# Kernel optimization log

Measured on AMD Instinct MI355X. Metric: run time of the kernel, lower is better.

The kernel has to match this reference:

```python
import jax, jax.numpy as jnp
import numpy as np

D_MODEL = 1024
NUM_HEAD = 16
D_K = D_MODEL // NUM_HEAD


def setup_inputs() -> dict:
    key = jax.random.key(0)
    ks = jax.random.split(key, 9)
    s = 1.0 / np.sqrt(D_MODEL)
    return {
        "x": jax.random.normal(ks[0], (2, 2048, D_MODEL), dtype=jnp.float32),
        "Wq": jax.random.normal(ks[1], (D_MODEL, D_MODEL), dtype=jnp.float32) * s,
        "bq": jax.random.normal(ks[2], (D_MODEL,), dtype=jnp.float32) * s,
        "Wk": jax.random.normal(ks[3], (D_MODEL, D_MODEL), dtype=jnp.float32) * s,
        "bk": jax.random.normal(ks[4], (D_MODEL,), dtype=jnp.float32) * s,
        "Wv": jax.random.normal(ks[5], (D_MODEL, D_MODEL), dtype=jnp.float32) * s,
        "bv": jax.random.normal(ks[6], (D_MODEL,), dtype=jnp.float32) * s,
        "Wo": jax.random.normal(ks[7], (D_MODEL, D_MODEL), dtype=jnp.float32) * s,
        "bo": jax.random.normal(ks[8], (D_MODEL,), dtype=jnp.float32) * s,
    }


def reference(x, Wq, bq, Wk, bk, Wv, bv, Wo, bo):
    B, S, _ = x.shape
    # QKV projections: [B,S,D] -> [B,H,S,d_k]
    def proj(W, b):
        y = jnp.einsum("bsd,df->bsf", x, W) + b
        return y.reshape(B, S, NUM_HEAD, D_K).transpose(0, 2, 1, 3)

    Q = proj(Wq, bq)
    K = proj(Wk, bk)
    V = proj(Wv, bv)
    scale = 1.0 / jnp.sqrt(jnp.asarray(D_K, dtype=x.dtype))
    attn = jnp.einsum("bhqd,bhkd->bhqk", Q, K) * scale  # [B,H,S,S]
    probs = jax.nn.softmax(attn, axis=-1)
    out = jnp.einsum("bhqk,bhkd->bhqd", probs, V)  # [B,H,S,d_k]
    out = out.transpose(0, 2, 1, 3).reshape(B, S, D_MODEL)
    return jnp.einsum("bsd,df->bsf", out, Wo) + bo
```

## Files before the change

kernel.cpp:

```cpp
#include <hip/hip_runtime.h>
#include <hip/hip_bf16.h>
#include <math.h>

constexpr int DM = 1024;
constexpr int NH = 16;
constexpr int DK = 64;
constexpr int SQ = 2048;
constexpr int BB = 2;
constexpr int MR = BB * SQ;

typedef short bf16x8 __attribute__((ext_vector_type(8)));
typedef float f32x4 __attribute__((ext_vector_type(4)));

__device__ inline unsigned short f2bf(float f) {
  unsigned u = __float_as_uint(f);
  unsigned r = (u + 0x7fffu + ((u >> 16) & 1u)) >> 16;
  return (unsigned short)r;
}

__device__ inline int fswz(int r) { return (r & 7) ^ ((r >> 3) & 7); }
__device__ inline int swz(int r, int c) {
  return r * 64 + ((((c >> 3) ^ fswz(r)) & 7) << 3) + (c & 7);
}

__global__ __launch_bounds__(256)
void cast_kernel(const float* __restrict__ in, unsigned short* __restrict__ out, int n8) {
  int i = blockIdx.x * 256 + threadIdx.x;
  if (i >= n8) return;
  float4 a = *(const float4*)&in[(size_t)i * 8];
  float4 b = *(const float4*)&in[(size_t)i * 8 + 4];
  ushort4 lo = {f2bf(a.x), f2bf(a.y), f2bf(a.z), f2bf(a.w)};
  ushort4 hi = {f2bf(b.x), f2bf(b.y), f2bf(b.z), f2bf(b.w)};
  *(ushort4*)&out[(size_t)i * 8] = lo;
  *(ushort4*)&out[(size_t)i * 8 + 4] = hi;
}

__global__ __launch_bounds__(256)
void transpose_cast_kernel(const float* __restrict__ W, unsigned short* __restrict__ Wt) {
  __shared__ float tl[32][33];
  const int tx = threadIdx.x & 31, ty = threadIdx.x >> 5;
  const int x0 = blockIdx.x * 32, y0 = blockIdx.y * 32;
  #pragma unroll
  for (int i = 0; i < 4; ++i)
    tl[ty + i * 8][tx] = W[(size_t)(y0 + ty + i * 8) * DM + x0 + tx];
  __syncthreads();
  #pragma unroll
  for (int i = 0; i < 4; ++i)
    Wt[(size_t)(x0 + ty + i * 8) * DM + y0 + tx] = f2bf(tl[tx][ty + i * 8]);
}

__global__ __launch_bounds__(256)
void concat_bias(const float* __restrict__ bq, const float* __restrict__ bk,
                 const float* __restrict__ bv, float* __restrict__ cb) {
  int i = blockIdx.x * 256 + threadIdx.x;
  if (i < 1024) cb[i] = bq[i];
  else if (i < 2048) cb[i] = bk[i - 1024];
  else if (i < 3072) cb[i] = bv[i - 2048];
}

__global__ __launch_bounds__(256)
void qkv_gemm(const unsigned short* __restrict__ A, const unsigned short* __restrict__ Wt3,
              const float* __restrict__ cbias, unsigned short* __restrict__ qkv)
{
  constexpr int K = DM;
  __shared__ unsigned short As[2][128 * 64];
  __shared__ unsigned short Bs[2][128 * 64];
  const int t = threadIdx.x;
  const int w = t >> 6, ln = t & 63;
  const int wr = w >> 1, wc = w & 1;
  const int rb = blockIdx.y * 128, cb = blockIdx.x * 128;

  f32x4 acc[4][4] = {};

  auto stage = [&](int buf, int k0) {
    #pragma unroll
    for (int j = 0; j < 4; ++j) {
      const int rows8 = (w * 4 + j) * 8;
      const int r = rows8 + (ln >> 3);
      const int gc = (((ln & 7) ^ fswz(r)) & 7) * 8;
      __builtin_amdgcn_global_load_lds(
          (const __attribute__((address_space(1))) void*)&A[(size_t)(rb + r) * K + k0 + gc],
          (__attribute__((address_space(3))) void*)&As[buf][rows8 * 64], 16, 0, 0);
      __builtin_amdgcn_global_load_lds(
          (const __attribute__((address_space(1))) void*)&Wt3[(size_t)(cb + r) * K + k0 + gc],
          (__attribute__((address_space(3))) void*)&Bs[buf][rows8 * 64], 16, 0, 0);
    }
  };

  stage(0, 0);
  asm volatile("s_waitcnt vmcnt(0)" ::: "memory");
  __builtin_amdgcn_s_barrier();

  for (int it = 0; it < K / 64; ++it) {
    const int buf = it & 1;
    if (it < K / 64 - 1) stage(buf ^ 1, (it + 1) * 64);
    const int rsel = ln & 15;
    #pragma unroll
    for (int kk = 0; kk < 2; ++kk) {
      const int ko = kk * 32 + (ln >> 4) * 8;
      bf16x8 af[4], bfr[4];
      #pragma unroll
      for (int m = 0; m < 4; ++m)
        af[m] = *(const bf16x8*)&As[buf][swz(wr * 64 + m * 16 + rsel, ko)];
      #pragma unroll
      for (int n = 0; n < 4; ++n)
        bfr[n] = *(const bf16x8*)&Bs[buf][swz(wc * 64 + n * 16 + rsel, ko)];
      #pragma unroll
      for (int m = 0; m < 4; ++m)
        #pragma unroll
        for (int n = 0; n < 4; ++n)
          acc[m][n] = __builtin_amdgcn_mfma_f32_16x16x32_bf16(af[m], bfr[n], acc[m][n], 0, 0, 0);
    }
    asm volatile("s_waitcnt vmcnt(0)" ::: "memory");
    __builtin_amdgcn_s_barrier();
  }

  const int cl = ln & 15, rg = (ln >> 4) * 4;
  const int which = cb >> 10;
  const float sc = (which == 0) ? 0.125f : 1.0f;
  unsigned short* dst0 = qkv + (size_t)which * MR * DM;
  #pragma unroll
  for (int m = 0; m < 4; ++m) {
    #pragma unroll
    for (int i = 0; i < 4; ++i) {
      const int r = rb + wr * 64 + m * 16 + rg + i;
      const int b = r >> 11, s = r & 2047;
      #pragma unroll
      for (int n = 0; n < 4; ++n) {
        const int c = cb + wc * 64 + n * 16 + cl;
        const float v = (acc[m][n][i] + cbias[c]) * sc;
        const int cc = c & 1023, h = cc >> 6, d = c & 63;
        dst0[(((size_t)(b * NH + h)) * SQ + s) * DK + d] = f2bf(v);
      }
    }
  }
}

__global__ __launch_bounds__(256)
void mfma_gemm_out(const unsigned short* __restrict__ A, const unsigned short* __restrict__ Bt,
                   const float* __restrict__ bias, float* __restrict__ outp)
{
  constexpr int K = DM, N = DM;
  __shared__ unsigned short As[2][128 * 64];
  __shared__ unsigned short Bs[2][128 * 64];
  const int t = threadIdx.x;
  const int w = t >> 6, ln = t & 63;
  const int wr = w >> 1, wc = w & 1;
  const int rb = blockIdx.y * 128, cb = blockIdx.x * 128;

  f32x4 acc[4][4] = {};

  auto stage = [&](int buf, int k0) {
    #pragma unroll
    for (int j = 0; j < 4; ++j) {
      const int rows8 = (w * 4 + j) * 8;
      const int r = rows8 + (ln >> 3);
      const int gc = (((ln & 7) ^ fswz(r)) & 7) * 8;
      __builtin_amdgcn_global_load_lds(
          (const __attribute__((address_space(1))) void*)&A[(size_t)(rb + r) * K + k0 + gc],
          (__attribute__((address_space(3))) void*)&As[buf][rows8 * 64], 16, 0, 0);
      __builtin_amdgcn_global_load_lds(
          (const __attribute__((address_space(1))) void*)&Bt[(size_t)(cb + r) * K + k0 + gc],
          (__attribute__((address_space(3))) void*)&Bs[buf][rows8 * 64], 16, 0, 0);
    }
  };

  stage(0, 0);
  asm volatile("s_waitcnt vmcnt(0)" ::: "memory");
  __builtin_amdgcn_s_barrier();

  for (int it = 0; it < K / 64; ++it) {
    const int buf = it & 1;
    if (it < K / 64 - 1) stage(buf ^ 1, (it + 1) * 64);
    const int rsel = ln & 15;
    #pragma unroll
    for (int kk = 0; kk < 2; ++kk) {
      const int ko = kk * 32 + (ln >> 4) * 8;
      bf16x8 af[4], bfr[4];
      #pragma unroll
      for (int m = 0; m < 4; ++m)
        af[m] = *(const bf16x8*)&As[buf][swz(wr * 64 + m * 16 + rsel, ko)];
      #pragma unroll
      for (int n = 0; n < 4; ++n)
        bfr[n] = *(const bf16x8*)&Bs[buf][swz(wc * 64 + n * 16 + rsel, ko)];
      #pragma unroll
      for (int m = 0; m < 4; ++m)
        #pragma unroll
        for (int n = 0; n < 4; ++n)
          acc[m][n] = __builtin_amdgcn_mfma_f32_16x16x32_bf16(af[m], bfr[n], acc[m][n], 0, 0, 0);
    }
    asm volatile("s_waitcnt vmcnt(0)" ::: "memory");
    __builtin_amdgcn_s_barrier();
  }

  const int cl = ln & 15, rg = (ln >> 4) * 4;
  #pragma unroll
  for (int m = 0; m < 4; ++m) {
    #pragma unroll
    for (int i = 0; i < 4; ++i) {
      const int r = rb + wr * 64 + m * 16 + rg + i;
      #pragma unroll
      for (int n = 0; n < 4; ++n) {
        const int c = cb + wc * 64 + n * 16 + cl;
        outp[(size_t)r * N + c] = acc[m][n][i] + bias[c];
      }
    }
  }
}

__global__ __launch_bounds__(512, 4)
void attn_mfma(const unsigned short* __restrict__ Qp, const unsigned short* __restrict__ Kp,
               const unsigned short* __restrict__ Vp, unsigned short* __restrict__ ctx)
{
  __shared__ unsigned short Qs[128 * 64];
  __shared__ unsigned short Ks[2][64 * 64];
  __shared__ unsigned short Vt[2][64 * 64];
  __shared__ unsigned short Pl[8 * 16 * 64];
  const int t = threadIdx.x, w = t >> 6, ln = t & 63;
  const int bh = blockIdx.y, q0 = blockIdx.x * 128;
  const unsigned short* Qb = Qp + (size_t)bh * SQ * DK;
  const unsigned short* Kb = Kp + (size_t)bh * SQ * DK;
  const unsigned short* Vb = Vp + (size_t)bh * SQ * DK;

  #pragma unroll
  for (int i = 0; i < 2; ++i) {
    int g = t + i * 512, r = g >> 3, cg = g & 7;
    uint4 qv = *(const uint4*)&Qb[(size_t)(q0 + r) * DK + cg * 8];
    *(uint4*)&Qs[r * 64 + (((cg ^ fswz(r)) & 7) << 3)] = qv;
  }
  __syncthreads();
  const int rsel = ln & 15, ko = (ln >> 4) * 8;
  bf16x8 qf[2];
  #pragma unroll
  for (int kw = 0; kw < 2; ++kw)
    qf[kw] = *(const bf16x8*)&Qs[swz(w * 16 + rsel, ko + 32 * kw)];

  f32x4 acc2[4] = {};
  float m = -1e30f, l = 0.f;

  const int r0 = t >> 3, cg0 = t & 7;
  const int ksl = r0 * 64 + (((cg0 ^ fswz(r0)) & 7) << 3);
  {
    uint4 kg = *(const uint4*)&Kb[(size_t)r0 * DK + cg0 * 8];
    uint4 vg = *(const uint4*)&Vb[(size_t)r0 * DK + cg0 * 8];
    *(uint4*)&Ks[0][ksl] = kg;
    const unsigned short* vv = (const unsigned short*)&vg;
    #pragma unroll
    for (int e = 0; e < 8; ++e)
      Vt[0][swz(cg0 * 8 + e, r0)] = vv[e];
  }
  __syncthreads();

  int cur = 0;
  for (int c0 = 0; c0 < SQ; c0 += 64) {
    const bool haveNext = (c0 + 64 < SQ);
    uint4 kg, vg;
    if (haveNext) {
      kg = *(const uint4*)&Kb[(size_t)(c0 + 64 + r0) * DK + cg0 * 8];
      vg = *(const uint4*)&Vb[(size_t)(c0 + 64 + r0) * DK + cg0 * 8];
    }

    f32x4 s[4] = {};
    __builtin_amdgcn_s_setprio(1);
    #pragma unroll
    for (int kw = 0; kw < 2; ++kw)
      #pragma unroll
      for (int fr = 0; fr < 4; ++fr) {
        bf16x8 kf = *(const bf16x8*)&Ks[cur][swz(fr * 16 + rsel, ko + 32 * kw)];
        s[fr] = __builtin_amdgcn_mfma_f32_16x16x32_bf16(kf, qf[kw], s[fr], 0, 0, 0);
      }
    __builtin_amdgcn_s_setprio(0);

    float t0 = fmaxf(fmaxf(s[0][0], s[0][1]), fmaxf(s[0][2], s[0][3]));
    float t1 = fmaxf(fmaxf(s[1][0], s[1][1]), fmaxf(s[1][2], s[1][3]));
    float t2 = fmaxf(fmaxf(s[2][0], s[2][1]), fmaxf(s[2][2], s[2][3]));
    float t3 = fmaxf(fmaxf(s[3][0], s[3][1]), fmaxf(s[3][2], s[3][3]));
    float tm = fmaxf(fmaxf(t0, t1), fmaxf(t2, t3));
    tm = fmaxf(tm, __shfl_xor(tm, 16));
    tm = fmaxf(tm, __shfl_xor(tm, 32));

    if (__any((tm - m) > 8.f)) {
      const float mnew = fmaxf(m, tm);
      const float corr = __expf(m - mnew);
      float ci[4];
      #pragma unroll
      for (int i = 0; i < 4; ++i) ci[i] = __shfl(corr, (ln >> 4) * 4 + i);
      #pragma unroll
      for (int n = 0; n < 4; ++n)
        #pragma unroll
        for (int i = 0; i < 4; ++i) acc2[n][i] *= ci[i];
      l *= corr;
      m = mnew;
    }

    float p[4][4];
    #pragma unroll
    for (int fr = 0; fr < 4; ++fr)
      #pragma unroll
      for (int i = 0; i < 4; ++i)
        p[fr][i] = __expf(s[fr][i] - m);
    float a0 = (p[0][0] + p[0][1]) + (p[0][2] + p[0][3]);
    float a1 = (p[1][0] + p[1][1]) + (p[1][2] + p[1][3]);
    float a2 = (p[2][0] + p[2][1]) + (p[2][2] + p[2][3]);
    float a3 = (p[3][0] + p[3][1]) + (p[3][2] + p[3][3]);
    float ps = (a0 + a1) + (a2 + a3);
    ps += __shfl_xor(ps, 16);
    ps += __shfl_xor(ps, 32);
    l += ps;

    #pragma unroll
    for (int fr = 0; fr < 4; ++fr) {
      unsigned r01, r23;
      asm("v_cvt_pk_bf16_f32 %0, %1, %2" : "=v"(r01) : "v"(p[fr][0]), "v"(p[fr][1]));
      asm("v_cvt_pk_bf16_f32 %0, %1, %2" : "=v"(r23) : "v"(p[fr][2]), "v"(p[fr][3]));
      uint2 pv = {r01, r23};
      const int kk0 = (ln >> 4) * 4 + fr * 16;
      *(uint2*)&Pl[w * 1024 + swz(rsel, kk0)] = pv;
    }

    __builtin_amdgcn_s_setprio(1);
    #pragma unroll
    for (int kw = 0; kw < 2; ++kw) {
      bf16x8 pf = *(const bf16x8*)&Pl[w * 1024 + swz(rsel, ko + 32 * kw)];
      #pragma unroll
      for (int n = 0; n < 4; ++n) {
        bf16x8 vf = *(const bf16x8*)&Vt[cur][swz(n * 16 + rsel, ko + 32 * kw)];
        acc2[n] = __builtin_amdgcn_mfma_f32_16x16x32_bf16(pf, vf, acc2[n], 0, 0, 0);
      }
    }
    __builtin_amdgcn_s_setprio(0);

    if (haveNext) {
      *(uint4*)&Ks[cur ^ 1][ksl] = kg;
      const unsigned short* vv = (const unsigned short*)&vg;
      #pragma unroll
      for (int e = 0; e < 8; ++e)
        Vt[cur ^ 1][swz(cg0 * 8 + e, r0)] = vv[e];
      __syncthreads();
    }
    cur ^= 1;
  }

  const float rl = 1.0f / l;
  float ri[4];
  #pragma unroll
  for (int i = 0; i < 4; ++i) ri[i] = __shfl(rl, (ln >> 4) * 4 + i);
  const int b = bh >> 4, h = bh & 15;
  #pragma unroll
  for (int n = 0; n < 4; ++n)
    #pragma unroll
    for (int i = 0; i < 4; ++i) {
      const int srow = q0 + w * 16 + (ln >> 4) * 4 + i;
      ctx[((size_t)(b * SQ + srow)) * DM + h * 64 + n * 16 + rsel] =
          f2bf(acc2[n][i] * ri[i]);
    }
}

extern "C" void kernel_launch(void* const* d_in, const int* in_sizes, int n_in,
                              void* d_out, int out_size, void* d_ws, size_t ws_size,
                              hipStream_t stream) {
  const float* x  = (const float*)d_in[0];
  const float* Wq = (const float*)d_in[1];
  const float* bq = (const float*)d_in[2];
  const float* Wk = (const float*)d_in[3];
  const float* bk = (const float*)d_in[4];
  const float* Wv = (const float*)d_in[5];
  const float* bv = (const float*)d_in[6];
  const float* Wo = (const float*)d_in[7];
  const float* bo = (const float*)d_in[8];
  float* out = (float*)d_out;

  unsigned short* xb    = (unsigned short*)d_ws;
  unsigned short* Wt3   = xb   + (size_t)MR * DM;
  unsigned short* Wto   = Wt3  + (size_t)3 * DM * DM;
  unsigned short* QKVb  = Wto  + (size_t)DM * DM;
  unsigned short* ctxb  = QKVb + (size_t)3 * MR * DM;
  float*          cbias = (float*)(ctxb + (size_t)MR * DM);

  cast_kernel<<<(MR * DM / 8 + 255) / 256, 256, 0, stream>>>(x, xb, MR * DM / 8);
  dim3 tg(DM / 32, DM / 32);
  transpose_cast_kernel<<<tg, 256, 0, stream>>>(Wq, Wt3);
  transpose_cast_kernel<<<tg, 256, 0, stream>>>(Wk, Wt3 + (size_t)DM * DM);
  transpose_cast_kernel<<<tg, 256, 0, stream>>>(Wv, Wt3 + (size_t)2 * DM * DM);
  transpose_cast_kernel<<<tg, 256, 0, stream>>>(Wo, Wto);
  concat_bias<<<12, 256, 0, stream>>>(bq, bk, bv, cbias);

  qkv_gemm<<<dim3(3 * DM / 128, MR / 128), 256, 0, stream>>>(xb, Wt3, cbias, QKVb);

  attn_mfma<<<dim3(SQ / 128, BB * NH), 512, 0, stream>>>(
      QKVb, QKVb + (size_t)MR * DM, QKVb + (size_t)2 * MR * DM, ctxb);

  mfma_gemm_out<<<dim3(DM / 128, MR / 128), 256, 0, stream>>>(ctxb, Wto, bo, out);
}
```

Baseline: 155.7 us.

## Rewrite attention with 32x32 MFMA, register-resident P, and pre-transposed V

Replaces the 16x16x32 attention kernel with one built on 32x32x16 bf16 MFMA. Each wave now owns 32 query rows and each block 256 queries. Probabilities are packed in registers and exchanged with v_permlane32_swap, so the LDS round trip for P is gone. A separate kernel pre-transposes V into global memory, which removes the scalar transposed LDS stores from the inner loop. K/V tiles are 256 keys wide with register prefetch, meaning fewer barriers per key. The costs are an extra kernel launch plus global traffic for V, and lower occupancy from the larger LDS tiles, single buffering and more registers.

```diff
diff --git a/kernel.cpp b/kernel.cpp
--- a/kernel.cpp
+++ b/kernel.cpp
@@ -11,6 +11,7 @@
 
 typedef short bf16x8 __attribute__((ext_vector_type(8)));
 typedef float f32x4 __attribute__((ext_vector_type(4)));
+typedef float f32x16 __attribute__((ext_vector_type(16)));
 
 __device__ inline unsigned short f2bf(float f) {
   unsigned u = __float_as_uint(f);
@@ -21,6 +22,11 @@
 __device__ inline int fswz(int r) { return (r & 7) ^ ((r >> 3) & 7); }
 __device__ inline int swz(int r, int c) {
   return r * 64 + ((((c >> 3) ^ fswz(r)) & 7) << 3) + (c & 7);
+}
+__device__ inline int vswz(int d, int c) {
+  int g = c >> 3;
+  g = (g & 24) | ((g ^ fswz(d)) & 7);
+  return d * 256 + g * 8 + (c & 7);
 }
 
 __global__ __launch_bounds__(256)
@@ -56,6 +62,32 @@
   if (i < 1024) cb[i] = bq[i];
   else if (i < 2048) cb[i] = bk[i - 1024];
   else if (i < 3072) cb[i] = bv[i - 2048];
+}
+
+__global__ __launch_bounds__(256)
+void transpose_v(const unsigned short* __restrict__ V, unsigned short* __restrict__ Vt) {
+  __shared__ unsigned short tl[64 * 64];
+  const int t = threadIdx.x;
+  const int s0 = blockIdx.x * 64, bh = blockIdx.y;
+  const unsigned short* src = V + (size_t)bh * SQ * DK;
+  unsigned short* dst = Vt + (size_t)bh * DK * SQ;
+  #pragma unroll
+  for (int i = 0; i < 2; ++i) {
+    int g = t + i * 256, r = g >> 3, cg = g & 7;
+    uint4 v = *(const uint4*)&src[(size_t)(s0 + r) * DK + cg * 8];
+    *(uint4*)&tl[r * 64 + (((cg ^ fswz(r)) & 7) << 3)] = v;
+  }
+  __syncthreads();
+  #pragma unroll
+  for (int i = 0; i < 2; ++i) {
+    int g = t + i * 256, d = g >> 3, cs = g & 7;
+    uint4 o;
+    unsigned short* op = (unsigned short*)&o;
+    #pragma unroll
+    for (int e = 0; e < 8; ++e)
+      op[e] = tl[swz(cs * 8 + e, d)];
+    *(uint4*)&dst[(size_t)d * SQ + s0 + cs * 8] = o;
+  }
 }
 
 __global__ __launch_bounds__(256)
@@ -208,152 +240,178 @@
   }
 }
 
-__global__ __launch_bounds__(512, 4)
-void attn_mfma(const unsigned short* __restrict__ Qp, const unsigned short* __restrict__ Kp,
-               const unsigned short* __restrict__ Vp, unsigned short* __restrict__ ctx)
+__global__ __launch_bounds__(512)
+void attn_mfma32(const unsigned short* __restrict__ Qp, const unsigned short* __restrict__ Kp,
+                 const unsigned short* __restrict__ VTp, unsigned short* __restrict__ ctx)
 {
-  __shared__ unsigned short Qs[128 * 64];
-  __shared__ unsigned short Ks[2][64 * 64];
-  __shared__ unsigned short Vt[2][64 * 64];
-  __shared__ unsigned short Pl[8 * 16 * 64];
+  __shared__ unsigned short Ks[256 * 64];
+  __shared__ unsigned short Vt[64 * 256];
   const int t = threadIdx.x, w = t >> 6, ln = t & 63;
-  const int bh = blockIdx.y, q0 = blockIdx.x * 128;
+  const int lh = ln >> 5;
+  const int bh = blockIdx.x, q0 = blockIdx.y * 256;
+  const int b = bh >> 4, h = bh & 15;
   const unsigned short* Qb = Qp + (size_t)bh * SQ * DK;
   const unsigned short* Kb = Kp + (size_t)bh * SQ * DK;
-  const unsigned short* Vb = Vp + (size_t)bh * SQ * DK;
-
-  #pragma unroll
-  for (int i = 0; i < 2; ++i) {
+  const unsigned short* Vb = VTp + (size_t)bh * DK * SQ;
+
+  #pragma unroll
+  for (int i = 0; i < 4; ++i) {
     int g = t + i * 512, r = g >> 3, cg = g & 7;
     uint4 qv = *(const uint4*)&Qb[(size_t)(q0 + r) * DK + cg * 8];
-    *(uint4*)&Qs[r * 64 + (((cg ^ fswz(r)) & 7) << 3)] = qv;
+    *(uint4*)&Ks[r * 64 + (((cg ^ fswz(r)) & 7) << 3)] = qv;
   }
   __syncthreads();
-  const int rsel = ln & 15, ko = (ln >> 4) * 8;
-  bf16x8 qf[2];
-  #pragma unroll
-  for (int kw = 0; kw < 2; ++kw)
-    qf[kw] = *(const bf16x8*)&Qs[swz(w * 16 + rsel, ko + 32 * kw)];
-
-  f32x4 acc2[4] = {};
+  bf16x8 qf[4];
+  #pragma unroll
+  for (int s = 0; s < 4; ++s)
+    qf[s] = *(const bf16x8*)&Ks[swz(w * 32 + (ln & 31), s * 16 + lh * 8)];
+  __syncthreads();
+
+  f32x16 o0 = {}, o1 = {};
   float m = -1e30f, l = 0.f;
 
-  const int r0 = t >> 3, cg0 = t & 7;
-  const int ksl = r0 * 64 + (((cg0 ^ fswz(r0)) & 7) << 3);
-  {
-    uint4 kg = *(const uint4*)&Kb[(size_t)r0 * DK + cg0 * 8];
-    uint4 vg = *(const uint4*)&Vb[(size_t)r0 * DK + cg0 * 8];
-    *(uint4*)&Ks[0][ksl] = kg;
-    const unsigned short* vv = (const unsigned short*)&vg;
-    #pragma unroll
-    for (int e = 0; e < 8; ++e)
-      Vt[0][swz(cg0 * 8 + e, r0)] = vv[e];
+  uint4 kr[4], vr[4];
+  #pragma unroll
+  for (int i = 0; i < 4; ++i) {
+    int g = t + i * 512;
+    kr[i] = *(const uint4*)&Kb[(size_t)(g >> 3) * DK + (g & 7) * 8];
+    vr[i] = *(const uint4*)&Vb[(size_t)(g >> 5) * SQ + (g & 31) * 8];
+  }
+  #pragma unroll
+  for (int i = 0; i < 4; ++i) {
+    int g = t + i * 512, r = g >> 3, cg = g & 7;
+    *(uint4*)&Ks[r * 64 + (((cg ^ fswz(r)) & 7) << 3)] = kr[i];
+    int d = g >> 5, c = g & 31;
+    *(uint4*)&Vt[d * 256 + (((c & 24) | ((c ^ fswz(d)) & 7)) << 3)] = vr[i];
   }
   __syncthreads();
 
-  int cur = 0;
-  for (int c0 = 0; c0 < SQ; c0 += 64) {
-    const bool haveNext = (c0 + 64 < SQ);
-    uint4 kg, vg;
-    if (haveNext) {
-      kg = *(const uint4*)&Kb[(size_t)(c0 + 64 + r0) * DK + cg0 * 8];
-      vg = *(const uint4*)&Vb[(size_t)(c0 + 64 + r0) * DK + cg0 * 8];
-    }
-
-    f32x4 s[4] = {};
-    __builtin_amdgcn_s_setprio(1);
-    #pragma unroll
-    for (int kw = 0; kw < 2; ++kw)
-      #pragma unroll
-      for (int fr = 0; fr < 4; ++fr) {
-        bf16x8 kf = *(const bf16x8*)&Ks[cur][swz(fr * 16 + rsel, ko + 32 * kw)];
-        s[fr] = __builtin_amdgcn_mfma_f32_16x16x32_bf16(kf, qf[kw], s[fr], 0, 0, 0);
-      }
-    __builtin_amdgcn_s_setprio(0);
-
-    float t0 = fmaxf(fmaxf(s[0][0], s[0][1]), fmaxf(s[0][2], s[0][3]));
-    float t1 = fmaxf(fmaxf(s[1][0], s[1][1]), fmaxf(s[1][2], s[1][3]));
-    float t2 = fmaxf(fmaxf(s[2][0], s[2][1]), fmaxf(s[2][2], s[2][3]));
-    float t3 = fmaxf(fmaxf(s[3][0], s[3][1]), fmaxf(s[3][2], s[3][3]));
-    float tm = fmaxf(fmaxf(t0, t1), fmaxf(t2, t3));
-    tm = fmaxf(tm, __shfl_xor(tm, 16));
-    tm = fmaxf(tm, __shfl_xor(tm, 32));
-
-    if (__any((tm - m) > 8.f)) {
-      const float mnew = fmaxf(m, tm);
-      const float corr = __expf(m - mnew);
-      float ci[4];
-      #pragma unroll
-      for (int i = 0; i < 4; ++i) ci[i] = __shfl(corr, (ln >> 4) * 4 + i);
-      #pragma unroll
-      for (int n = 0; n < 4; ++n)
+  for (int oc = 0; oc < SQ / 256; ++oc) {
+    const bool nxt = (oc + 1) < SQ / 256;
+    if (nxt) {
+      const int base = (oc + 1) * 256;
+      #pragma unroll
+      for (int i = 0; i < 4; ++i) {
+        int g = t + i * 512;
+        kr[i] = *(const uint4*)&Kb[(size_t)(base + (g >> 3)) * DK + (g & 7) * 8];
+        vr[i] = *(const uint4*)&Vb[(size_t)(g >> 5) * SQ + base + (g & 31) * 8];
+      }
+    }
+
+    #pragma unroll
+    for (int it = 0; it < 4; ++it) {
+      f32x16 s0 = {}, s1 = {};
+      __builtin_amdgcn_s_setprio(1);
+      #pragma unroll
+      for (int s = 0; s < 4; ++s) {
+        bf16x8 k0 = *(const bf16x8*)&Ks[swz(it * 64 + (ln & 31), s * 16 + lh * 8)];
+        bf16x8 k1 = *(const bf16x8*)&Ks[swz(it * 64 + 32 + (ln & 31), s * 16 + lh * 8)];
+        s0 = __builtin_amdgcn_mfma_f32_32x32x16_bf16(k0, qf[s], s0, 0, 0, 0);
+        s1 = __builtin_amdgcn_mfma_f32_32x32x16_bf16(k1, qf[s], s1, 0, 0, 0);
+      }
+      __builtin_amdgcn_s_setprio(0);
+
+      float mx0 = fmaxf(s0[0], s0[1]), mx1 = fmaxf(s0[2], s0[3]);
+      #pragma unroll
+      for (int j = 4; j < 16; j += 4) {
+        mx0 = fmaxf(mx0, fmaxf(s0[j], s0[j + 1]));
+        mx1 = fmaxf(mx1, fmaxf(s0[j + 2], s0[j + 3]));
+      }
+      #pragma unroll
+      for (int j = 0; j < 16; j += 4) {
+        mx0 = fmaxf(mx0, fmaxf(s1[j], s1[j + 1]));
+        mx1 = fmaxf(mx1, fmaxf(s1[j + 2], s1[j + 3]));
+      }
+      float tm = fmaxf(mx0, mx1);
+      tm = fmaxf(tm, __shfl_xor(tm, 32));
+
+      if (__any((tm - m) > 8.f)) {
+        const float mnew = fmaxf(m, tm);
+        const float corr = __expf(m - mnew);
+        float ci[16];
         #pragma unroll
-        for (int i = 0; i < 4; ++i) acc2[n][i] *= ci[i];
-      l *= corr;
-      m = mnew;
-    }
-
-    float p[4][4];
-    #pragma unroll
-    for (int fr = 0; fr < 4; ++fr)
-      #pragma unroll
-      for (int i = 0; i < 4; ++i)
-        p[fr][i] = __expf(s[fr][i] - m);
-    float a0 = (p[0][0] + p[0][1]) + (p[0][2] + p[0][3]);
-    float a1 = (p[1][0] + p[1][1]) + (p[1][2] + p[1][3]);
-    float a2 = (p[2][0] + p[2][1]) + (p[2][2] + p[2][3]);
-    float a3 = (p[3][0] + p[3][1]) + (p[3][2] + p[3][3]);
-    float ps = (a0 + a1) + (a2 + a3);
-    ps += __shfl_xor(ps, 16);
-    ps += __shfl_xor(ps, 32);
-    l += ps;
-
-    #pragma unroll
-    for (int fr = 0; fr < 4; ++fr) {
-      unsigned r01, r23;
-      asm("v_cvt_pk_bf16_f32 %0, %1, %2" : "=v"(r01) : "v"(p[fr][0]), "v"(p[fr][1]));
-      asm("v_cvt_pk_bf16_f32 %0, %1, %2" : "=v"(r23) : "v"(p[fr][2]), "v"(p[fr][3]));
-      uint2 pv = {r01, r23};
-      const int kk0 = (ln >> 4) * 4 + fr * 16;
-      *(uint2*)&Pl[w * 1024 + swz(rsel, kk0)] = pv;
-    }
-
-    __builtin_amdgcn_s_setprio(1);
-    #pragma unroll
-    for (int kw = 0; kw < 2; ++kw) {
-      bf16x8 pf = *(const bf16x8*)&Pl[w * 1024 + swz(rsel, ko + 32 * kw)];
-      #pragma unroll
-      for (int n = 0; n < 4; ++n) {
-        bf16x8 vf = *(const bf16x8*)&Vt[cur][swz(n * 16 + rsel, ko + 32 * kw)];
-        acc2[n] = __builtin_amdgcn_mfma_f32_16x16x32_bf16(pf, vf, acc2[n], 0, 0, 0);
-      }
-    }
-    __builtin_amdgcn_s_setprio(0);
-
-    if (haveNext) {
-      *(uint4*)&Ks[cur ^ 1][ksl] = kg;
-      const unsigned short* vv = (const unsigned short*)&vg;
-      #pragma unroll
-      for (int e = 0; e < 8; ++e)
-        Vt[cur ^ 1][swz(cg0 * 8 + e, r0)] = vv[e];
+        for (int j = 0; j < 16; ++j)
+          ci[j] = __shfl(corr, (j & 3) + 8 * (j >> 2) + 4 * lh);
+        #pragma unroll
+        for (int j = 0; j < 16; ++j) { o0[j] *= ci[j]; o1[j] *= ci[j]; }
+        l *= corr;
+        m = mnew;
+      }
+
+      float p0[16], p1[16];
+      #pragma unroll
+      for (int j = 0; j < 16; ++j) {
+        p0[j] = __expf(s0[j] - m);
+        p1[j] = __expf(s1[j] - m);
+      }
+      float ps = 0.f;
+      #pragma unroll
+      for (int j = 0; j < 16; ++j) ps += p0[j] + p1[j];
+      ps += __shfl_xor(ps, 32);
+      l += ps;
+
+      __builtin_amdgcn_s_setprio(1);
+      #pragma unroll
+      for (int s = 0; s < 4; ++s) {
+        unsigned w0, w1, w2, w3;
+        if (s == 0) {
+          asm("v_cvt_pk_bf16_f32 %0, %1, %2" : "=v"(w0) : "v"(p0[0]), "v"(p0[1]));
+          asm("v_cvt_pk_bf16_f32 %0, %1, %2" : "=v"(w1) : "v"(p0[2]), "v"(p0[3]));
+          asm("v_cvt_pk_bf16_f32 %0, %1, %2" : "=v"(w2) : "v"(p0[4]), "v"(p0[5]));
+          asm("v_cvt_pk_bf16_f32 %0, %1, %2" : "=v"(w3) : "v"(p0[6]), "v"(p0[7]));
+        } else if (s == 1) {
+          asm("v_cvt_pk_bf16_f32 %0, %1, %2" : "=v"(w0) : "v"(p0[8]), "v"(p0[9]));
+          asm("v_cvt_pk_bf16_f32 %0, %1, %2" : "=v"(w1) : "v"(p0[10]), "v"(p0[11]));
+          asm("v_cvt_pk_bf16_f32 %0, %1, %2" : "=v"(w2) : "v"(p0[12]), "v"(p0[13]));
+          asm("v_cvt_pk_bf16_f32 %0, %1, %2" : "=v"(w3) : "v"(p0[14]), "v"(p0[15]));
+        } else if (s == 2) {
+          asm("v_cvt_pk_bf16_f32 %0, %1, %2" : "=v"(w0) : "v"(p1[0]), "v"(p1[1]));
+          asm("v_cvt_pk_bf16_f32 %0, %1, %2" : "=v"(w1) : "v"(p1[2]), "v"(p1[3]));
+          asm("v_cvt_pk_bf16_f32 %0, %1, %2" : "=v"(w2) : "v"(p1[4]), "v"(p1[5]));
+          asm("v_cvt_pk_bf16_f32 %0, %1, %2" : "=v"(w3) : "v"(p1[6]), "v"(p1[7]));
+        } else {
+          asm("v_cvt_pk_bf16_f32 %0, %1, %2" : "=v"(w0) : "v"(p1[8]), "v"(p1[9]));
+          asm("v_cvt_pk_bf16_f32 %0, %1, %2" : "=v"(w1) : "v"(p1[10]), "v"(p1[11]));
+          asm("v_cvt_pk_bf16_f32 %0, %1, %2" : "=v"(w2) : "v"(p1[12]), "v"(p1[13]));
+          asm("v_cvt_pk_bf16_f32 %0, %1, %2" : "=v"(w3) : "v"(p1[14]), "v"(p1[15]));
+        }
+        asm("v_permlane32_swap_b32 %0, %1" : "+v"(w0), "+v"(w2));
+        asm("v_permlane32_swap_b32 %0, %1" : "+v"(w1), "+v"(w3));
+        union { unsigned u[4]; bf16x8 v; } pa;
+        pa.u[0] = w0; pa.u[1] = w1; pa.u[2] = w2; pa.u[3] = w3;
+        bf16x8 v0 = *(const bf16x8*)&Vt[vswz(ln & 31, it * 64 + s * 16 + lh * 8)];
+        bf16x8 v1 = *(const bf16x8*)&Vt[vswz(32 + (ln & 31), it * 64 + s * 16 + lh * 8)];
+        o0 = __builtin_amdgcn_mfma_f32_32x32x16_bf16(pa.v, v0, o0, 0, 0, 0);
+        o1 = __builtin_amdgcn_mfma_f32_32x32x16_bf16(pa.v, v1, o1, 0, 0, 0);
+      }
+      __builtin_amdgcn_s_setprio(0);
+    }
+
+    __syncthreads();
+    if (nxt) {
+      #pragma unroll
+      for (int i = 0; i < 4; ++i) {
+        int g = t + i * 512, r = g >> 3, cg = g & 7;
+        *(uint4*)&Ks[r * 64 + (((cg ^ fswz(r)) & 7) << 3)] = kr[i];
+        int d = g >> 5, c = g & 31;
+        *(uint4*)&Vt[d * 256 + (((c & 24) | ((c ^ fswz(d)) & 7)) << 3)] = vr[i];
+      }
       __syncthreads();
     }
-    cur ^= 1;
   }
 
   const float rl = 1.0f / l;
-  float ri[4];
-  #pragma unroll
-  for (int i = 0; i < 4; ++i) ri[i] = __shfl(rl, (ln >> 4) * 4 + i);
-  const int b = bh >> 4, h = bh & 15;
-  #pragma unroll
-  for (int n = 0; n < 4; ++n)
-    #pragma unroll
-    for (int i = 0; i < 4; ++i) {
-      const int srow = q0 + w * 16 + (ln >> 4) * 4 + i;
-      ctx[((size_t)(b * SQ + srow)) * DM + h * 64 + n * 16 + rsel] =
-          f2bf(acc2[n][i] * ri[i]);
-    }
+  float ri[16];
+  #pragma unroll
+  for (int j = 0; j < 16; ++j)
+    ri[j] = __shfl(rl, (j & 3) + 8 * (j >> 2) + 4 * lh);
+  #pragma unroll
+  for (int j = 0; j < 16; ++j) {
+    const int srow = q0 + w * 32 + (j & 3) + 8 * (j >> 2) + 4 * lh;
+    unsigned short* dst = ctx + ((size_t)(b * SQ + srow)) * DM + h * 64;
+    dst[(ln & 31)]      = f2bf(o0[j] * ri[j]);
+    dst[32 + (ln & 31)] = f2bf(o1[j] * ri[j]);
+  }
 }
 
 extern "C" void kernel_launch(void* const* d_in, const int* in_sizes, int n_in,
@@ -374,7 +432,8 @@
   unsigned short* Wt3   = xb   + (size_t)MR * DM;
   unsigned short* Wto   = Wt3  + (size_t)3 * DM * DM;
   unsigned short* QKVb  = Wto  + (size_t)DM * DM;
-  unsigned short* ctxb  = QKVb + (size_t)3 * MR * DM;
+  unsigned short* Vtb   = QKVb + (size_t)3 * MR * DM;
+  unsigned short* ctxb  = Vtb  + (size_t)MR * DM;
   float*          cbias = (float*)(ctxb + (size_t)MR * DM);
 
   cast_kernel<<<(MR * DM / 8 + 255) / 256, 256, 0, stream>>>(x, xb, MR * DM / 8);
@@ -386,9 +445,11 @@
   concat_bias<<<12, 256, 0, stream>>>(bq, bk, bv, cbias);
 
   qkv_gemm<<<dim3(3 * DM / 128, MR / 128), 256, 0, stream>>>(xb, Wt3, cbias, QKVb);
-
-  attn_mfma<<<dim3(SQ / 128, BB * NH), 512, 0, stream>>>(
-      QKVb, QKVb + (size_t)MR * DM, QKVb + (size_t)2 * MR * DM, ctxb);
+  transpose_v<<<dim3(SQ / 64, BB * NH), 256, 0, stream>>>(
+      QKVb + (size_t)2 * MR * DM, Vtb);
+
+  attn_mfma32<<<dim3(BB * NH, SQ / 256), 512, 0, stream>>>(
+      QKVb, QKVb + (size_t)MR * DM, Vtb, ctxb);
 
   mfma_gemm_out<<<dim3(DM / 128, MR / 128), 256, 0, stream>>>(ctxb, Wto, bo, out);
 }
```

Result: slower. 170.0 us (+9.2%).

## Pre-transpose V globally, widen attention K/V tiles to 128, merge prep kernels

Applied to the files above, without the earlier changes.

Adds a transpose_v kernel that writes V in [bh, d, s] layout, so the attention kernel loads V^T with vectorized 16-byte stores instead of eight scalar transposing LDS writes per thread. The attention loop now stages 128-key tiles in a single buffer with register prefetch, giving two sub-iterations per barrier pair instead of one. The four weight transpose launches are merged into one grid-z launch, and the bias concat kernel is dropped in favour of reading the bias pointers directly. The costs are an extra kernel launch plus an extra global round-trip for V, and the launch-bounds occupancy hint on the attention kernel is removed.

```diff
diff --git a/kernel.cpp b/kernel.cpp
--- a/kernel.cpp
+++ b/kernel.cpp
@@ -22,6 +22,7 @@
 __device__ inline int swz(int r, int c) {
   return r * 64 + ((((c >> 3) ^ fswz(r)) & 7) << 3) + (c & 7);
 }
+__device__ inline int vslot(int d, int g) { return (g & 8) | ((g ^ fswz(d)) & 7); }
 
 __global__ __launch_bounds__(256)
 void cast_kernel(const float* __restrict__ in, unsigned short* __restrict__ out, int n8) {
@@ -36,8 +37,13 @@
 }
 
 __global__ __launch_bounds__(256)
-void transpose_cast_kernel(const float* __restrict__ W, unsigned short* __restrict__ Wt) {
+void transpose_cast_all(const float* __restrict__ Wq, const float* __restrict__ Wk,
+                        const float* __restrict__ Wv, const float* __restrict__ Wo,
+                        unsigned short* __restrict__ Wt3, unsigned short* __restrict__ Wto) {
   __shared__ float tl[32][33];
+  const int z = blockIdx.z;
+  const float* W = (z == 0) ? Wq : (z == 1) ? Wk : (z == 2) ? Wv : Wo;
+  unsigned short* Wt = (z < 3) ? (Wt3 + (size_t)z * DM * DM) : Wto;
   const int tx = threadIdx.x & 31, ty = threadIdx.x >> 5;
   const int x0 = blockIdx.x * 32, y0 = blockIdx.y * 32;
   #pragma unroll
@@ -50,17 +56,35 @@
 }
 
 __global__ __launch_bounds__(256)
-void concat_bias(const float* __restrict__ bq, const float* __restrict__ bk,
-                 const float* __restrict__ bv, float* __restrict__ cb) {
-  int i = blockIdx.x * 256 + threadIdx.x;
-  if (i < 1024) cb[i] = bq[i];
-  else if (i < 2048) cb[i] = bk[i - 1024];
-  else if (i < 3072) cb[i] = bv[i - 2048];
+void transpose_v(const unsigned short* __restrict__ V, unsigned short* __restrict__ Vt) {
+  __shared__ unsigned short tl[64 * 64];
+  const int t = threadIdx.x;
+  const int s0 = blockIdx.x * 64, bh = blockIdx.y;
+  const unsigned short* src = V + (size_t)bh * SQ * DK;
+  unsigned short* dst = Vt + (size_t)bh * DK * SQ;
+  #pragma unroll
+  for (int i = 0; i < 2; ++i) {
+    int g = t + i * 256, r = g >> 3, cg = g & 7;
+    uint4 v = *(const uint4*)&src[(size_t)(s0 + r) * DK + cg * 8];
+    *(uint4*)&tl[r * 64 + (((cg ^ fswz(r)) & 7) << 3)] = v;
+  }
+  __syncthreads();
+  #pragma unroll
+  for (int i = 0; i < 2; ++i) {
+    int g = t + i * 256, d = g >> 3, cs = g & 7;
+    uint4 o;
+    unsigned short* op = (unsigned short*)&o;
+    #pragma unroll
+    for (int e = 0; e < 8; ++e)
+      op[e] = tl[swz(cs * 8 + e, d)];
+    *(uint4*)&dst[(size_t)d * SQ + s0 + cs * 8] = o;
+  }
 }
 
 __global__ __launch_bounds__(256)
 void qkv_gemm(const unsigned short* __restrict__ A, const unsigned short* __restrict__ Wt3,
-              const float* __restrict__ cbias, unsigned short* __restrict__ qkv)
+              const float* __restrict__ bq, const float* __restrict__ bk,
+              const float* __restrict__ bv, unsigned short* __restrict__ qkv)
 {
   constexpr int K = DM;
   __shared__ unsigned short As[2][128 * 64];
@@ -118,6 +142,7 @@
   const int cl = ln & 15, rg = (ln >> 4) * 4;
   const int which = cb >> 10;
   const float sc = (which == 0) ? 0.125f : 1.0f;
+  const float* bp = (which == 0) ? bq : (which == 1) ? bk : bv;
   unsigned short* dst0 = qkv + (size_t)which * MR * DM;
   #pragma unroll
   for (int m = 0; m < 4; ++m) {
@@ -128,8 +153,8 @@
       #pragma unroll
       for (int n = 0; n < 4; ++n) {
         const int c = cb + wc * 64 + n * 16 + cl;
-        const float v = (acc[m][n][i] + cbias[c]) * sc;
         const int cc = c & 1023, h = cc >> 6, d = c & 63;
+        const float v = (acc[m][n][i] + bp[cc]) * sc;
         dst0[(((size_t)(b * NH + h)) * SQ + s) * DK + d] = f2bf(v);
       }
     }
@@ -208,19 +233,19 @@
   }
 }
 
-__global__ __launch_bounds__(512, 4)
+__global__ __launch_bounds__(512)
 void attn_mfma(const unsigned short* __restrict__ Qp, const unsigned short* __restrict__ Kp,
-               const unsigned short* __restrict__ Vp, unsigned short* __restrict__ ctx)
+               const unsigned short* __restrict__ VTp, unsigned short* __restrict__ ctx)
 {
   __shared__ unsigned short Qs[128 * 64];
-  __shared__ unsigned short Ks[2][64 * 64];
-  __shared__ unsigned short Vt[2][64 * 64];
+  __shared__ unsigned short Ks[128 * 64];
+  __shared__ unsigned short Vt[64 * 128];
   __shared__ unsigned short Pl[8 * 16 * 64];
   const int t = threadIdx.x, w = t >> 6, ln = t & 63;
   const int bh = blockIdx.y, q0 = blockIdx.x * 128;
   const unsigned short* Qb = Qp + (size_t)bh * SQ * DK;
   const unsigned short* Kb = Kp + (size_t)bh * SQ * DK;
-  const unsigned short* Vb = Vp + (size_t)bh * SQ * DK;
+  const unsigned short* Vb = VTp + (size_t)bh * DK * SQ;
 
   #pragma unroll
   for (int i = 0; i < 2; ++i) {
@@ -238,107 +263,108 @@
   f32x4 acc2[4] = {};
   float m = -1e30f, l = 0.f;
 
-  const int r0 = t >> 3, cg0 = t & 7;
-  const int ksl = r0 * 64 + (((cg0 ^ fswz(r0)) & 7) << 3);
-  {
-    uint4 kg = *(const uint4*)&Kb[(size_t)r0 * DK + cg0 * 8];
-    uint4 vg = *(const uint4*)&Vb[(size_t)r0 * DK + cg0 * 8];
-    *(uint4*)&Ks[0][ksl] = kg;
-    const unsigned short* vv = (const unsigned short*)&vg;
-    #pragma unroll
-    for (int e = 0; e < 8; ++e)
-      Vt[0][swz(cg0 * 8 + e, r0)] = vv[e];
-  }
-  __syncthreads();
-
-  int cur = 0;
-  for (int c0 = 0; c0 < SQ; c0 += 64) {
-    const bool haveNext = (c0 + 64 < SQ);
-    uint4 kg, vg;
-    if (haveNext) {
-      kg = *(const uint4*)&Kb[(size_t)(c0 + 64 + r0) * DK + cg0 * 8];
-      vg = *(const uint4*)&Vb[(size_t)(c0 + 64 + r0) * DK + cg0 * 8];
-    }
-
-    f32x4 s[4] = {};
-    __builtin_amdgcn_s_setprio(1);
-    #pragma unroll
-    for (int kw = 0; kw < 2; ++kw)
+  uint4 kg[2], vg[2];
+  #pragma unroll
+  for (int i = 0; i < 2; ++i) {
+    int g = t + i * 512;
+    kg[i] = *(const uint4*)&Kb[(size_t)(g >> 3) * DK + (g & 7) * 8];
+    vg[i] = *(const uint4*)&Vb[(size_t)(g >> 4) * SQ + (g & 15) * 8];
+  }
+
+  for (int c0 = 0; c0 < SQ; c0 += 128) {
+    __syncthreads();
+    #pragma unroll
+    for (int i = 0; i < 2; ++i) {
+      int g = t + i * 512;
+      int r = g >> 3, cg = g & 7;
+      *(uint4*)&Ks[r * 64 + (((cg ^ fswz(r)) & 7) << 3)] = kg[i];
+      int d = g >> 4, c = g & 15;
+      *(uint4*)&Vt[d * 128 + vslot(d, c) * 8] = vg[i];
+    }
+    __syncthreads();
+
+    if (c0 + 128 < SQ) {
+      #pragma unroll
+      for (int i = 0; i < 2; ++i) {
+        int g = t + i * 512;
+        kg[i] = *(const uint4*)&Kb[(size_t)(c0 + 128 + (g >> 3)) * DK + (g & 7) * 8];
+        vg[i] = *(const uint4*)&Vb[(size_t)(g >> 4) * SQ + c0 + 128 + (g & 15) * 8];
+      }
+    }
+
+    #pragma unroll
+    for (int it = 0; it < 2; ++it) {
+      f32x4 s[4] = {};
+      __builtin_amdgcn_s_setprio(1);
+      #pragma unroll
+      for (int kw = 0; kw < 2; ++kw)
+        #pragma unroll
+        for (int fr = 0; fr < 4; ++fr) {
+          bf16x8 kf = *(const bf16x8*)&Ks[swz(it * 64 + fr * 16 + rsel, ko + 32 * kw)];
+          s[fr] = __builtin_amdgcn_mfma_f32_16x16x32_bf16(kf, qf[kw], s[fr], 0, 0, 0);
+        }
+      __builtin_amdgcn_s_setprio(0);
+
+      float t0 = fmaxf(fmaxf(s[0][0], s[0][1]), fmaxf(s[0][2], s[0][3]));
+      float t1 = fmaxf(fmaxf(s[1][0], s[1][1]), fmaxf(s[1][2], s[1][3]));
+      float t2 = fmaxf(fmaxf(s[2][0], s[2][1]), fmaxf(s[2][2], s[2][3]));
+      float t3 = fmaxf(fmaxf(s[3][0], s[3][1]), fmaxf(s[3][2], s[3][3]));
+      float tm = fmaxf(fmaxf(t0, t1), fmaxf(t2, t3));
+      tm = fmaxf(tm, __shfl_xor(tm, 16));
+      tm = fmaxf(tm, __shfl_xor(tm, 32));
+
+      if (__any((tm - m) > 8.f)) {
+        const float mnew = fmaxf(m, tm);
+        const float corr = __expf(m - mnew);
+        float ci[4];
+        #pragma unroll
+        for (int i = 0; i < 4; ++i) ci[i] = __shfl(corr, (ln >> 4) * 4 + i);
+        #pragma unroll
+        for (int n = 0; n < 4; ++n)
+          #pragma unroll
+          for (int i = 0; i < 4; ++i) acc2[n][i] *= ci[i];
+        l *= corr;
+        m = mnew;
+      }
+
+      #pragma unroll
+      for (int fr = 0; fr < 4; ++fr)
+        #pragma unroll
+        for (int i = 0; i < 4; ++i)
+          s[fr][i] = __expf(s[fr][i] - m);
+      float a0 = (s[0][0] + s[0][1]) + (s[0][2] + s[0][3]);
+      float a1 = (s[1][0] + s[1][1]) + (s[1][2] + s[1][3]);
+      float a2 = (s[2][0] + s[2][1]) + (s[2][2] + s[2][3]);
+      float a3 = (s[3][0] + s[3][1]) + (s[3][2] + s[3][3]);
+      float ps = (a0 + a1) + (a2 + a3);
+      ps += __shfl_xor(ps, 16);
+      ps += __shfl_xor(ps, 32);
+      l += ps;
+
       #pragma unroll
       for (int fr = 0; fr < 4; ++fr) {
-        bf16x8 kf = *(const bf16x8*)&Ks[cur][swz(fr * 16 + rsel, ko + 32 * kw)];
-        s[fr] = __builtin_amdgcn_mfma_f32_16x16x32_bf16(kf, qf[kw], s[fr], 0, 0, 0);
-      }
-    __builtin_amdgcn_s_setprio(0);
-
-    float t0 = fmaxf(fmaxf(s[0][0], s[0][1]), fmaxf(s[0][2], s[0][3]));
-    float t1 = fmaxf(fmaxf(s[1][0], s[1][1]), fmaxf(s[1][2], s[1][3]));
-    float t2 = fmaxf(fmaxf(s[2][0], s[2][1]), fmaxf(s[2][2], s[2][3]));
-    float t3 = fmaxf(fmaxf(s[3][0], s[3][1]), fmaxf(s[3][2], s[3][3]));
-    float tm = fmaxf(fmaxf(t0, t1), fmaxf(t2, t3));
-    tm = fmaxf(tm, __shfl_xor(tm, 16));
-    tm = fmaxf(tm, __shfl_xor(tm, 32));
-
-    if (__any((tm - m) > 8.f)) {
-      const float mnew = fmaxf(m, tm);
-      const float corr = __expf(m - mnew);
-      float ci[4];
-      #pragma unroll
-      for (int i = 0; i < 4; ++i) ci[i] = __shfl(corr, (ln >> 4) * 4 + i);
-      #pragma unroll
-      for (int n = 0; n < 4; ++n)
-        #pragma unroll
-        for (int i = 0; i < 4; ++i) acc2[n][i] *= ci[i];
-      l *= corr;
-      m = mnew;
-    }
-
-    float p[4][4];
-    #pragma unroll
-    for (int fr = 0; fr < 4; ++fr)
-      #pragma unroll
-      for (int i = 0; i < 4; ++i)
-        p[fr][i] = __expf(s[fr][i] - m);
-    float a0 = (p[0][0] + p[0][1]) + (p[0][2] + p[0][3]);
-    float a1 = (p[1][0] + p[1][1]) + (p[1][2] + p[1][3]);
-    float a2 = (p[2][0] + p[2][1]) + (p[2][2] + p[2][3]);
-    float a3 = (p[3][0] + p[3][1]) + (p[3][2] + p[3][3]);
-    float ps = (a0 + a1) + (a2 + a3);
-    ps += __shfl_xor(ps, 16);
-    ps += __shfl_xor(ps, 32);
-    l += ps;
-
-    #pragma unroll
-    for (int fr = 0; fr < 4; ++fr) {
-      unsigned r01, r23;
-      asm("v_cvt_pk_bf16_f32 %0, %1, %2" : "=v"(r01) : "v"(p[fr][0]), "v"(p[fr][1]));
-      asm("v_cvt_pk_bf16_f32 %0, %1, %2" : "=v"(r23) : "v"(p[fr][2]), "v"(p[fr][3]));
-      uint2 pv = {r01, r23};
-      const int kk0 = (ln >> 4) * 4 + fr * 16;
-      *(uint2*)&Pl[w * 1024 + swz(rsel, kk0)] = pv;
-    }
-
-    __builtin_amdgcn_s_setprio(1);
-    #pragma unroll
-    for (int kw = 0; kw < 2; ++kw) {
-      bf16x8 pf = *(const bf16x8*)&Pl[w * 1024 + swz(rsel, ko + 32 * kw)];
-      #pragma unroll
-      for (int n = 0; n < 4; ++n) {
-        bf16x8 vf = *(const bf16x8*)&Vt[cur][swz(n * 16 + rsel, ko + 32 * kw)];
-        acc2[n] = __builtin_amdgcn_mfma_f32_16x16x32_bf16(pf, vf, acc2[n], 0, 0, 0);
-      }
-    }
-    __builtin_amdgcn_s_setprio(0);
-
-    if (haveNext) {
-      *(uint4*)&Ks[cur ^ 1][ksl] = kg;
-      const unsigned short* vv = (const unsigned short*)&vg;
-      #pragma unroll
-      for (int e = 0; e < 8; ++e)
-        Vt[cur ^ 1][swz(cg0 * 8 + e, r0)] = vv[e];
-      __syncthreads();
-    }
-    cur ^= 1;
+        unsigned r01, r23;
+        asm("v_cvt_pk_bf16_f32 %0, %1, %2" : "=v"(r01) : "v"(s[fr][0]), "v"(s[fr][1]));
+        asm("v_cvt_pk_bf16_f32 %0, %1, %2" : "=v"(r23) : "v"(s[fr][2]), "v"(s[fr][3]));
+        uint2 pv = {r01, r23};
+        const int kk0 = (ln >> 4) * 4 + fr * 16;
+        *(uint2*)&Pl[w * 1024 + swz(rsel, kk0)] = pv;
+      }
+
+      __builtin_amdgcn_s_setprio(1);
+      #pragma unroll
+      for (int kw = 0; kw < 2; ++kw) {
+        bf16x8 pf = *(const bf16x8*)&Pl[w * 1024 + swz(rsel, ko + 32 * kw)];
+        #pragma unroll
+        for (int n = 0; n < 4; ++n) {
+          const int d = n * 16 + rsel;
+          const int gx = it * 8 + (ln >> 4) + 4 * kw;
+          bf16x8 vf = *(const bf16x8*)&Vt[d * 128 + vslot(d, gx) * 8];
+          acc2[n] = __builtin_amdgcn_mfma_f32_16x16x32_bf16(pf, vf, acc2[n], 0, 0, 0);
+        }
+      }
+      __builtin_amdgcn_s_setprio(0);
+    }
   }
 
   const float rl = 1.0f / l;
@@ -374,21 +400,20 @@
   unsigned short* Wt3   = xb   + (size_t)MR * DM;
   unsigned short* Wto   = Wt3  + (size_t)3 * DM * DM;
   unsigned short* QKVb  = Wto  + (size_t)DM * DM;
-  unsigned short* ctxb  = QKVb + (size_t)3 * MR * DM;
-  float*          cbias = (float*)(ctxb + (size_t)MR * DM);
+  unsigned short* Vtb   = QKVb + (size_t)3 * MR * DM;
+  unsigned short* ctxb  = Vtb  + (size_t)MR * DM;
 
   cast_kernel<<<(MR * DM / 8 + 255) / 256, 256, 0, stream>>>(x, xb, MR * DM / 8);
-  dim3 tg(DM / 32, DM / 32);
-  transpose_cast_kernel<<<tg, 256, 0, stream>>>(Wq, Wt3);
-  transpose_cast_kernel<<<tg, 256, 0, stream>>>(Wk, Wt3 + (size_t)DM * DM);
-  transpose_cast_kernel<<<tg, 256, 0, stream>>>(Wv, Wt3 + (size_t)2 * DM * DM);
-  transpose_cast_kernel<<<tg, 256, 0, stream>>>(Wo, Wto);
-  concat_bias<<<12, 256, 0, stream>>>(bq, bk, bv, cbias);
-
-  qkv_gemm<<<dim3(3 * DM / 128, MR / 128), 256, 0, stream>>>(xb, Wt3, cbias, QKVb);
+  transpose_cast_all<<<dim3(DM / 32, DM / 32, 4), 256, 0, stream>>>(
+      Wq, Wk, Wv, Wo, Wt3, Wto);
+
+  qkv_gemm<<<dim3(3 * DM / 128, MR / 128), 256, 0, stream>>>(
+      xb, Wt3, bq, bk, bv, QKVb);
+  transpose_v<<<dim3(SQ / 64, BB * NH), 256, 0, stream>>>(
+      QKVb + (size_t)2 * MR * DM, Vtb);
 
   attn_mfma<<<dim3(SQ / 128, BB * NH), 512, 0, stream>>>(
-      QKVb, QKVb + (size_t)MR * DM, QKVb + (size_t)2 * MR * DM, ctxb);
+      QKVb, QKVb + (size_t)MR * DM, Vtb, ctxb);
 
   mfma_gemm_out<<<dim3(DM / 128, MR / 128), 256, 0, stream>>>(ctxb, Wto, bo, out);
 }
```

After: 168.1 us. 1.08x slower.

## Merge weight transpose launches, drop bias concat, single-buffer attention K/V tiles

Applied to the files above, without the earlier changes.

The four weight transpose-cast launches become one launch that selects the matrix from blockIdx.z. The bias-concatenation kernel is removed and the QKV GEMM epilogue reads bq/bk/bv directly, which cuts launch overhead. The attention kernel moves from double-buffered to single-buffered K/V shared tiles with two barriers per iteration, while still prefetching the next tile into registers. This lowers LDS use and may raise occupancy, but it adds a barrier per iteration and may expose LDS write latency.

```diff
diff --git a/kernel.cpp b/kernel.cpp
--- a/kernel.cpp
+++ b/kernel.cpp
@@ -36,8 +36,13 @@
 }
 
 __global__ __launch_bounds__(256)
-void transpose_cast_kernel(const float* __restrict__ W, unsigned short* __restrict__ Wt) {
+void transpose_cast_all(const float* __restrict__ Wq, const float* __restrict__ Wk,
+                        const float* __restrict__ Wv, const float* __restrict__ Wo,
+                        unsigned short* __restrict__ Wt3, unsigned short* __restrict__ Wto) {
   __shared__ float tl[32][33];
+  const int z = blockIdx.z;
+  const float* W = (z == 0) ? Wq : (z == 1) ? Wk : (z == 2) ? Wv : Wo;
+  unsigned short* Wt = (z < 3) ? (Wt3 + (size_t)z * DM * DM) : Wto;
   const int tx = threadIdx.x & 31, ty = threadIdx.x >> 5;
   const int x0 = blockIdx.x * 32, y0 = blockIdx.y * 32;
   #pragma unroll
@@ -50,17 +55,9 @@
 }
 
 __global__ __launch_bounds__(256)
-void concat_bias(const float* __restrict__ bq, const float* __restrict__ bk,
-                 const float* __restrict__ bv, float* __restrict__ cb) {
-  int i = blockIdx.x * 256 + threadIdx.x;
-  if (i < 1024) cb[i] = bq[i];
-  else if (i < 2048) cb[i] = bk[i - 1024];
-  else if (i < 3072) cb[i] = bv[i - 2048];
-}
-
-__global__ __launch_bounds__(256)
 void qkv_gemm(const unsigned short* __restrict__ A, const unsigned short* __restrict__ Wt3,
-              const float* __restrict__ cbias, unsigned short* __restrict__ qkv)
+              const float* __restrict__ bq, const float* __restrict__ bk,
+              const float* __restrict__ bv, unsigned short* __restrict__ qkv)
 {
   constexpr int K = DM;
   __shared__ unsigned short As[2][128 * 64];
@@ -118,6 +115,7 @@
   const int cl = ln & 15, rg = (ln >> 4) * 4;
   const int which = cb >> 10;
   const float sc = (which == 0) ? 0.125f : 1.0f;
+  const float* bp = (which == 0) ? bq : (which == 1) ? bk : bv;
   unsigned short* dst0 = qkv + (size_t)which * MR * DM;
   #pragma unroll
   for (int m = 0; m < 4; ++m) {
@@ -128,8 +126,8 @@
       #pragma unroll
       for (int n = 0; n < 4; ++n) {
         const int c = cb + wc * 64 + n * 16 + cl;
-        const float v = (acc[m][n][i] + cbias[c]) * sc;
         const int cc = c & 1023, h = cc >> 6, d = c & 63;
+        const float v = (acc[m][n][i] + bp[cc]) * sc;
         dst0[(((size_t)(b * NH + h)) * SQ + s) * DK + d] = f2bf(v);
       }
     }
@@ -213,8 +211,8 @@
                const unsigned short* __restrict__ Vp, unsigned short* __restrict__ ctx)
 {
   __shared__ unsigned short Qs[128 * 64];
-  __shared__ unsigned short Ks[2][64 * 64];
-  __shared__ unsigned short Vt[2][64 * 64];
+  __shared__ unsigned short Ks[64 * 64];
+  __shared__ unsigned short Vt[64 * 64];
   __shared__ unsigned short Pl[8 * 16 * 64];
   const int t = threadIdx.x, w = t >> 6, ln = t & 63;
   const int bh = blockIdx.y, q0 = blockIdx.x * 128;
@@ -239,23 +237,22 @@
   float m = -1e30f, l = 0.f;
 
   const int r0 = t >> 3, cg0 = t & 7;
-  const int ksl = r0 * 64 + (((cg0 ^ fswz(r0)) & 7) << 3);
-  {
-    uint4 kg = *(const uint4*)&Kb[(size_t)r0 * DK + cg0 * 8];
-    uint4 vg = *(const uint4*)&Vb[(size_t)r0 * DK + cg0 * 8];
-    *(uint4*)&Ks[0][ksl] = kg;
-    const unsigned short* vv = (const unsigned short*)&vg;
-    #pragma unroll
-    for (int e = 0; e < 8; ++e)
-      Vt[0][swz(cg0 * 8 + e, r0)] = vv[e];
-  }
-  __syncthreads();
-
-  int cur = 0;
+  uint4 kg = *(const uint4*)&Kb[(size_t)r0 * DK + cg0 * 8];
+  uint4 vg = *(const uint4*)&Vb[(size_t)r0 * DK + cg0 * 8];
+
   for (int c0 = 0; c0 < SQ; c0 += 64) {
-    const bool haveNext = (c0 + 64 < SQ);
-    uint4 kg, vg;
-    if (haveNext) {
+    __syncthreads();
+    *(uint4*)&Ks[r0 * 64 + (((cg0 ^ fswz(r0)) & 7) << 3)] = kg;
+    {
+      const unsigned short* vv = (const unsigned short*)&vg;
+      const int d0 = cg0 * 8;
+      #pragma unroll
+      for (int e = 0; e < 8; ++e)
+        Vt[swz(d0 + e, r0)] = vv[e];
+    }
+    __syncthreads();
+
+    if (c0 + 64 < SQ) {
       kg = *(const uint4*)&Kb[(size_t)(c0 + 64 + r0) * DK + cg0 * 8];
       vg = *(const uint4*)&Vb[(size_t)(c0 + 64 + r0) * DK + cg0 * 8];
     }
@@ -266,7 +263,7 @@
     for (int kw = 0; kw < 2; ++kw)
       #pragma unroll
       for (int fr = 0; fr < 4; ++fr) {
-        bf16x8 kf = *(const bf16x8*)&Ks[cur][swz(fr * 16 + rsel, ko + 32 * kw)];
+        bf16x8 kf = *(const bf16x8*)&Ks[swz(fr * 16 + rsel, ko + 32 * kw)];
         s[fr] = __builtin_amdgcn_mfma_f32_16x16x32_bf16(kf, qf[kw], s[fr], 0, 0, 0);
       }
     __builtin_amdgcn_s_setprio(0);
@@ -324,21 +321,11 @@
       bf16x8 pf = *(const bf16x8*)&Pl[w * 1024 + swz(rsel, ko + 32 * kw)];
       #pragma unroll
       for (int n = 0; n < 4; ++n) {
-        bf16x8 vf = *(const bf16x8*)&Vt[cur][swz(n * 16 + rsel, ko + 32 * kw)];
+        bf16x8 vf = *(const bf16x8*)&Vt[swz(n * 16 + rsel, ko + 32 * kw)];
         acc2[n] = __builtin_amdgcn_mfma_f32_16x16x32_bf16(pf, vf, acc2[n], 0, 0, 0);
       }
     }
     __builtin_amdgcn_s_setprio(0);
-
-    if (haveNext) {
-      *(uint4*)&Ks[cur ^ 1][ksl] = kg;
-      const unsigned short* vv = (const unsigned short*)&vg;
-      #pragma unroll
-      for (int e = 0; e < 8; ++e)
-        Vt[cur ^ 1][swz(cg0 * 8 + e, r0)] = vv[e];
-      __syncthreads();
-    }
-    cur ^= 1;
   }
 
   const float rl = 1.0f / l;
@@ -375,17 +362,13 @@
   unsigned short* Wto   = Wt3  + (size_t)3 * DM * DM;
   unsigned short* QKVb  = Wto  + (size_t)DM * DM;
   unsigned short* ctxb  = QKVb + (size_t)3 * MR * DM;
-  float*          cbias = (float*)(ctxb + (size_t)MR * DM);
 
   cast_kernel<<<(MR * DM / 8 + 255) / 256, 256, 0, stream>>>(x, xb, MR * DM / 8);
-  dim3 tg(DM / 32, DM / 32);
-  transpose_cast_kernel<<<tg, 256, 0, stream>>>(Wq, Wt3);
-  transpose_cast_kernel<<<tg, 256, 0, stream>>>(Wk, Wt3 + (size_t)DM * DM);
-  transpose_cast_kernel<<<tg, 256, 0, stream>>>(Wv, Wt3 + (size_t)2 * DM * DM);
-  transpose_cast_kernel<<<tg, 256, 0, stream>>>(Wo, Wto);
-  concat_bias<<<12, 256, 0, stream>>>(bq, bk, bv, cbias);
-
-  qkv_gemm<<<dim3(3 * DM / 128, MR / 128), 256, 0, stream>>>(xb, Wt3, cbias, QKVb);
+  transpose_cast_all<<<dim3(DM / 32, DM / 32, 4), 256, 0, stream>>>(
+      Wq, Wk, Wv, Wo, Wt3, Wto);
+
+  qkv_gemm<<<dim3(3 * DM / 128, MR / 128), 256, 0, stream>>>(
+      xb, Wt3, bq, bk, bv, QKVb);
 
   attn_mfma<<<dim3(SQ / 128, BB * NH), 512, 0, stream>>>(
       QKVb, QKVb + (size_t)MR * DM, QKVb + (size_t)2 * MR * DM, ctxb);
```

New measurement: 145.7 us. -6.4%, faster.
